# Kernel tuning notes

Hardware: AMD Instinct MI355X
Metric: run time of the kernel (lower is better)

The kernel has to match this reference:

```python
import jax, jax.numpy as jnp
import numpy as np

TAU = 0.6      # critical_fractile from params()
GAMMA = 0.1    # L2-regularization weight (init arg)
N_ITERS = 60   # bisection iterations (machine precision on [0,1])
EPS = 1e-12

# The cvxpy problem per sample (prob vector p over support y):
#   min_z  p @ pinball(y - z) + GAMMA * ||p * (y - z)||_2,   0 <= z <= 1
# with pinball(e) = max(TAU*e, (TAU-1)*e). This is a 1-D convex problem in z;
# we solve the stationarity condition g(z) = df/dz = 0 by bisection (g is
# nondecreasing), then take one Newton step at the root so implicit gradients
# w.r.t. p flow correctly (dz/dp = -(dg/dp)/(dg/dz)). Fully batched over B.

def setup_inputs() -> dict:
    key = jax.random.key(0)
    B, S = 32768, 1001
    x = jax.random.uniform(key, (B, S), dtype=jnp.float32)
    x = x / x.sum(-1, keepdims=True)                      # probability vectors
    y_supp = jnp.linspace(0.0, 1.0, S, dtype=jnp.float32)  # support grid
    return {"x": x, "y_supp": y_supp}


def _grad_z(z, p, y):
    """g(z)=df/dz and its z-derivative, batched. z:[B], p:[B,S], y:[S]."""
    e = y[None, :] - z[:, None]                                  # [B,S]
    pin = jnp.sum(p * jnp.where(e >= 0, -TAU, 1.0 - TAU), -1)    # d(pinball)/dz
    pe = p * e
    nrm = jnp.sqrt(jnp.sum(pe * pe, -1) + EPS)                   # ||p*e||
    s1 = jnp.sum(p * p * e, -1)
    g = pin - GAMMA * s1 / nrm
    gp = GAMMA * (jnp.sum(p * p, -1) / nrm - (s1 * s1) / (nrm ** 3))
    return g, gp


def _solve(x, y):
    B = x.shape[0]
    p0 = jax.lax.stop_gradient(x)
    y0 = jax.lax.stop_gradient(y)
    lo = jnp.zeros((B,), x.dtype)
    hi = jnp.ones((B,), x.dtype)

    def body(carry, _):
        lo, hi = carry
        mid = 0.5 * (lo + hi)
        g, _ = _grad_z(mid, p0, y0)
        lo = jnp.where(g < 0, mid, lo)
        hi = jnp.where(g < 0, hi, mid)
        return (lo, hi), None

    (lo, hi), _ = jax.lax.scan(body, (lo, hi), None, length=N_ITERS)
    z0 = jax.lax.stop_gradient(0.5 * (lo + hi))
    # one Newton step at the root -> correct implicit gradients w.r.t. x, y
    g, gp = _grad_z(z0, x, y)
    z = z0 - g / jnp.maximum(gp, 1e-8)
    # boundary clamp (minimum at 0 or 1 if g doesn't change sign)
    g0, _ = _grad_z(jnp.zeros((B,), x.dtype), p0, y0)
    g1, _ = _grad_z(jnp.ones((B,), x.dtype), p0, y0)
    z = jnp.where(g0 >= 0, 0.0, jnp.where(g1 <= 0, 1.0, jnp.clip(z, 0.0, 1.0)))
    return z


def reference(x, y_supp):
    z = _solve(x, y_supp)                   # [B]
    e = y_supp[None, :] - z[:, None]        # error variable, [B,S]
    pinball = jnp.maximum(TAU * e, (TAU - 1.0) * e)  # pinball_loss at optimum
    w_error = x * e                          # w_error variable
    return (z[:, None], pinball, e, w_error)
```

## Files before the change

kernel.cpp:

```cpp
#include <hip/hip_runtime.h>
#include <hip/hip_bf16.h>


constexpr int NS   = 1001;
constexpr int SPAD = 1024;
constexpr int NT   = 256;

__global__ __launch_bounds__(NT) void newsvendor_kernel(
    const float* __restrict__ x,
    const float* __restrict__ ysup,
    float* __restrict__ out,
    int B)
{
    __shared__ float  sp[SPAD];
    __shared__ float  sy[SPAD];
    __shared__ double scdf[SPAD];
    __shared__ double wred[12];
    __shared__ double wtot[4];
    __shared__ int    wredi[4];
    __shared__ double bc[4];
    __shared__ float  zf_sh;

    const int row  = blockIdx.x;
    const int tid  = threadIdx.x;
    const int lane = tid & 63;
    const int wv   = tid >> 6;
    const float* xr = x + (size_t)row * NS;

    for (int i = tid; i < SPAD; i += NT) {
        sp[i] = (i < NS) ? xr[i]   : 0.0f;
        sy[i] = (i < NS) ? ysup[i] : 2.0f;
    }
    __syncthreads();

    double a = 0.0, b1 = 0.0, c2 = 0.0;
    for (int i = tid; i < NS; i += NT) {
        double p = (double)sp[i], y = (double)sy[i];
        double pp = p * p;
        a += pp; b1 += pp * y; c2 += pp * (y * y);
    }
    for (int off = 32; off > 0; off >>= 1) {
        a  += __shfl_xor(a,  off);
        b1 += __shfl_xor(b1, off);
        c2 += __shfl_xor(c2, off);
    }
    if (lane == 0) { wred[wv*3+0] = a; wred[wv*3+1] = b1; wred[wv*3+2] = c2; }

    const int base = tid * 4;
    double p0 = sp[base], p1 = sp[base+1], p2 = sp[base+2], p3 = sp[base+3];
    double l0 = 0.0, l1 = p0, l2 = p0+p1, l3 = p0+p1+p2;
    double s  = p0+p1+p2+p3;
    double inc = s;
    for (int d = 1; d < 64; d <<= 1) {
        double t = __shfl_up(inc, (unsigned)d);
        if (lane >= d) inc += t;
    }
    if (lane == 63) wtot[wv] = inc;
    __syncthreads();

    double woff = 0.0;
    for (int w = 0; w < wv; ++w) woff += wtot[w];
    double ebase = woff + (inc - s);
    scdf[base]   = ebase + l0;
    scdf[base+1] = ebase + l1;
    scdf[base+2] = ebase + l2;
    scdf[base+3] = ebase + l3;
    if (tid == 0) {
        bc[0] = wred[0]+wred[3]+wred[6]+wred[9];
        bc[1] = wred[1]+wred[4]+wred[7]+wred[10];
        bc[2] = wred[2]+wred[5]+wred[8]+wred[11];
    }
    __syncthreads();

    const double A    = bc[0], B1 = bc[1], C = bc[2];
    const double Pt   = scdf[NS];
    const double ca   = (double)0.6f;
    const double cb   = (double)0.4f;
    const double cab  = ca + cb;
    const double GA   = (double)0.1f;
    const double GA2  = GA * GA;
    const double EPSd = (double)1e-12f;

    int kmin = 0x7fffffff;
    for (int k = tid; k < NS; k += NT) {
        double z  = (double)sy[k];
        double t  = cab * scdf[k] - ca * Pt;
        double s1 = B1 - z * A;
        double qe = C - z * (2.0 * B1 - z * A) + EPSd;
        double lq = t * t * qe, rq = GA2 * s1 * s1;
        bool ge = (t >= 0.0) ? (s1 <= 0.0 || lq >= rq)
                             : (s1 <  0.0 && lq <= rq);
        if (ge) kmin = min(kmin, k);
    }
    for (int off = 32; off > 0; off >>= 1)
        kmin = min(kmin, __shfl_xor(kmin, off));
    if (lane == 0) wredi[wv] = kmin;
    __syncthreads();

    if (tid == 0) {
        int kstar = min(min(wredi[0], wredi[1]), min(wredi[2], wredi[3]));

        double g0 = -ca * Pt - GA * B1 / sqrt(C + EPSd);
        int c1 = (sy[NS-1] < 1.0f) ? NS : NS - 1;
        double s1b = B1 - A;
        double qe1 = C - (2.0 * B1 - A) + EPSd;
        double g1 = cab * scdf[c1] - ca * Pt - GA * s1b / sqrt(qe1);

        float zf;
        if (g0 >= 0.0)      zf = 0.0f;
        else if (g1 <= 0.0) zf = 1.0f;
        else {
            int kk = kstar;
            float zlF, zrF;
            if (kk >= NS) { kk = NS; zlF = sy[NS-1]; zrF = 1.0f; }
            else {
                zlF = (kk > 0) ? sy[kk-1] : 0.0f;
                zrF = sy[kk];
            }
            double Phat = cab * scdf[kk] - ca * Pt;

            double zl  = (double)zlF;
            double s1l = B1 - zl * A;
            double qel = C - zl * (2.0 * B1 - zl * A) + EPSd;
            double lql = Phat * Phat * qel, rql = GA2 * s1l * s1l;
            bool Flge = (Phat >= 0.0) ? (s1l <= 0.0 || lql >= rql)
                                      : (s1l <  0.0 && lql <= rql);

            bool   jumpc;
            double zeta;
            if (Flge) { jumpc = true; zeta = zl; }
            else {
                jumpc = false;
                double E  = (C * A - B1 * B1) + A * EPSd;
                double cc = Phat / (GA * sqrt(A));
                double u  = cc * sqrt(E / fmax(1.0 - cc * cc, 1e-300));
                zeta = (B1 - u) / A;
                zeta = fmin(fmax(zeta, zl), (double)zrF);
            }

            float flo = 0.0f, fhi = 1.0f;
            for (int it = 0; it < 60; ++it) {
                float mid = 0.5f * (flo + fhi);
                bool dec = jumpc ? (mid <= zlF) : ((double)mid < zeta);
                if (dec) flo = mid; else fhi = mid;
            }
            float z0 = 0.5f * (flo + fhi);

            int cnt = (kk - 1) + ((zlF < z0) ? 1 : 0) + ((zrF < z0) ? 1 : 0);
            if (cnt < 0) cnt = 0;

            double z0d = (double)z0;
            double s1 = B1 - z0d * A;
            double qe = C - z0d * (2.0 * B1 - z0d * A) + EPSd;
            double nr = sqrt(qe);
            double inv = 1.0 / nr;
            double g  = cab * scdf[cnt] - ca * Pt - GA * s1 * inv;
            double gp = GA * inv * (A - s1 * s1 * (inv * inv));
            double zn = z0d - g / fmax(gp, (double)1e-8f);
            zn = fmin(fmax(zn, 0.0), 1.0);
            zf = (float)zn;
        }
        zf_sh = zf;
    }
    __syncthreads();

    const float zf = zf_sh;
    const size_t Bz = (size_t)B;
    const size_t rb = (size_t)row * NS;
    float* outPin = out + Bz + rb;
    float* outE   = out + Bz + Bz * NS + rb;
    float* outW   = out + Bz + 2 * Bz * NS + rb;
    if (tid == 0) out[row] = zf;
    for (int i = tid; i < NS; i += NT) {
        float e  = sy[i] - zf;
        float pb = fmaxf(0.6f * e, -0.4f * e);
        outPin[i] = pb;
        outE[i]   = e;
        outW[i]   = sp[i] * e;
    }
}

extern "C" void kernel_launch(void* const* d_in, const int* in_sizes, int n_in,
                              void* d_out, int out_size, void* d_ws, size_t ws_size,
                              hipStream_t stream)
{
    const float* x = (const float*)d_in[0];
    const float* y = (const float*)d_in[1];
    float* out = (float*)d_out;
    const int Ssz = in_sizes[1];
    const int B   = in_sizes[0] / Ssz;
    newsvendor_kernel<<<B, NT, 0, stream>>>(x, y, out, B);
}
```

Measured before the change: 551.4 us.

## Fuse reductions into per-thread float4 pass, pad scdf, drop a barrier, nontemporal stores

Each thread now loads its four elements of p and y once as float4 and computes both the moment sums and the prefix-scan inputs from those registers. The kink search evaluates those same four candidates from registers instead of re-reading shared memory. The bc broadcast and one __syncthreads are removed: every thread reads the warp partials directly. The scdf array is padded to avoid bank conflicts, the scalar bisection exits early at a float fixed point, and output writes use nontemporal stores. The kernel is dominated by memory traffic, so the compute-side savings may matter little. Nontemporal stores could help or hurt the write-back path.

```diff
diff --git a/kernel.cpp b/kernel.cpp
--- a/kernel.cpp
+++ b/kernel.cpp
@@ -2,9 +2,10 @@
 #include <hip/hip_bf16.h>
 
 
-constexpr int NS   = 1001;
-constexpr int SPAD = 1024;
-constexpr int NT   = 256;
+constexpr int NS = 1001;
+constexpr int SP = 1024;
+constexpr int NT = 256;
+#define SIDX(i) ((i) + ((i) >> 2))
 
 __global__ __launch_bounds__(NT) void newsvendor_kernel(
     const float* __restrict__ x,
@@ -12,13 +13,12 @@
     float* __restrict__ out,
     int B)
 {
-    __shared__ float  sp[SPAD];
-    __shared__ float  sy[SPAD];
-    __shared__ double scdf[SPAD];
+    __shared__ float  sp[SP];
+    __shared__ float  sy[SP];
+    __shared__ double scdf[SP + SP/4];
     __shared__ double wred[12];
     __shared__ double wtot[4];
     __shared__ int    wredi[4];
-    __shared__ double bc[4];
     __shared__ float  zf_sh;
 
     const int row  = blockIdx.x;
@@ -27,18 +27,26 @@
     const int wv   = tid >> 6;
     const float* xr = x + (size_t)row * NS;
 
-    for (int i = tid; i < SPAD; i += NT) {
+    #pragma unroll
+    for (int j = 0; j < 4; ++j) {
+        int i = tid + j * NT;
         sp[i] = (i < NS) ? xr[i]   : 0.0f;
         sy[i] = (i < NS) ? ysup[i] : 2.0f;
     }
     __syncthreads();
 
-    double a = 0.0, b1 = 0.0, c2 = 0.0;
-    for (int i = tid; i < NS; i += NT) {
-        double p = (double)sp[i], y = (double)sy[i];
-        double pp = p * p;
-        a += pp; b1 += pp * y; c2 += pp * (y * y);
-    }
+    const int base = tid * 4;
+    float4 pf = *reinterpret_cast<const float4*>(&sp[base]);
+    float4 yf = *reinterpret_cast<const float4*>(&sy[base]);
+    double p0 = pf.x, p1 = pf.y, p2 = pf.z, p3 = pf.w;
+    double y0d = yf.x, y1d = yf.y, y2d = yf.z, y3d = yf.w;
+    double q0 = p0*p0, q1 = p1*p1, q2 = p2*p2, q3 = p3*p3;
+    double a  = ((q0 + q1) + q2) + q3;
+    double b1 = ((q0*y0d + q1*y1d) + q2*y2d) + q3*y3d;
+    double c2 = ((q0*y0d*y0d + q1*y1d*y1d) + q2*y2d*y2d) + q3*y3d*y3d;
+    double l1 = p0, l2 = p0 + p1, l3 = l2 + p2;
+    double s  = l3 + p3;
+
     for (int off = 32; off > 0; off >>= 1) {
         a  += __shfl_xor(a,  off);
         b1 += __shfl_xor(b1, off);
@@ -46,10 +54,6 @@
     }
     if (lane == 0) { wred[wv*3+0] = a; wred[wv*3+1] = b1; wred[wv*3+2] = c2; }
 
-    const int base = tid * 4;
-    double p0 = sp[base], p1 = sp[base+1], p2 = sp[base+2], p3 = sp[base+3];
-    double l0 = 0.0, l1 = p0, l2 = p0+p1, l3 = p0+p1+p2;
-    double s  = p0+p1+p2+p3;
     double inc = s;
     for (int d = 1; d < 64; d <<= 1) {
         double t = __shfl_up(inc, (unsigned)d);
@@ -58,22 +62,19 @@
     if (lane == 63) wtot[wv] = inc;
     __syncthreads();
 
-    double woff = 0.0;
-    for (int w = 0; w < wv; ++w) woff += wtot[w];
-    double ebase = woff + (inc - s);
-    scdf[base]   = ebase + l0;
-    scdf[base+1] = ebase + l1;
-    scdf[base+2] = ebase + l2;
-    scdf[base+3] = ebase + l3;
-    if (tid == 0) {
-        bc[0] = wred[0]+wred[3]+wred[6]+wred[9];
-        bc[1] = wred[1]+wred[4]+wred[7]+wred[10];
-        bc[2] = wred[2]+wred[5]+wred[8]+wred[11];
-    }
-    __syncthreads();
-
-    const double A    = bc[0], B1 = bc[1], C = bc[2];
-    const double Pt   = scdf[NS];
+    const double w0 = wtot[0], w1 = wtot[1], w2 = wtot[2], w3 = wtot[3];
+    const double Pt = ((w0 + w1) + w2) + w3;
+    const double A  = wred[0] + wred[3] + wred[6] + wred[9];
+    const double B1 = wred[1] + wred[4] + wred[7] + wred[10];
+    const double C  = wred[2] + wred[5] + wred[8] + wred[11];
+    double woff = (wv > 0 ? w0 : 0.0) + (wv > 1 ? w1 : 0.0) + (wv > 2 ? w2 : 0.0);
+    double eb   = woff + (inc - s);
+    double sc0 = eb, sc1 = eb + l1, sc2 = eb + l2, sc3 = eb + l3;
+    scdf[SIDX(base+0)] = sc0;
+    scdf[SIDX(base+1)] = sc1;
+    scdf[SIDX(base+2)] = sc2;
+    scdf[SIDX(base+3)] = sc3;
+
     const double ca   = (double)0.6f;
     const double cb   = (double)0.4f;
     const double cab  = ca + cb;
@@ -82,15 +83,21 @@
     const double EPSd = (double)1e-12f;
 
     int kmin = 0x7fffffff;
-    for (int k = tid; k < NS; k += NT) {
-        double z  = (double)sy[k];
-        double t  = cab * scdf[k] - ca * Pt;
-        double s1 = B1 - z * A;
-        double qe = C - z * (2.0 * B1 - z * A) + EPSd;
-        double lq = t * t * qe, rq = GA2 * s1 * s1;
-        bool ge = (t >= 0.0) ? (s1 <= 0.0 || lq >= rq)
-                             : (s1 <  0.0 && lq <= rq);
-        if (ge) kmin = min(kmin, k);
+    {
+        double zz[4] = { y0d, y1d, y2d, y3d };
+        double cd[4] = { sc0, sc1, sc2, sc3 };
+        #pragma unroll
+        for (int j = 0; j < 4; ++j) {
+            int k = base + j;
+            double z  = zz[j];
+            double t  = cab * cd[j] - ca * Pt;
+            double s1 = B1 - z * A;
+            double qe = C - z * (2.0 * B1 - z * A) + EPSd;
+            double lq = t * t * qe, rq = GA2 * s1 * s1;
+            bool ge = (t >= 0.0) ? (s1 <= 0.0 || lq >= rq)
+                                 : (s1 <  0.0 && lq <= rq);
+            if (k < NS && ge) kmin = min(kmin, k);
+        }
     }
     for (int off = 32; off > 0; off >>= 1)
         kmin = min(kmin, __shfl_xor(kmin, off));
@@ -104,7 +111,7 @@
         int c1 = (sy[NS-1] < 1.0f) ? NS : NS - 1;
         double s1b = B1 - A;
         double qe1 = C - (2.0 * B1 - A) + EPSd;
-        double g1 = cab * scdf[c1] - ca * Pt - GA * s1b / sqrt(qe1);
+        double g1 = cab * scdf[SIDX(c1)] - ca * Pt - GA * s1b / sqrt(qe1);
 
         float zf;
         if (g0 >= 0.0)      zf = 0.0f;
@@ -117,7 +124,7 @@
                 zlF = (kk > 0) ? sy[kk-1] : 0.0f;
                 zrF = sy[kk];
             }
-            double Phat = cab * scdf[kk] - ca * Pt;
+            double Phat = cab * scdf[SIDX(kk)] - ca * Pt;
 
             double zl  = (double)zlF;
             double s1l = B1 - zl * A;
@@ -142,7 +149,9 @@
             for (int it = 0; it < 60; ++it) {
                 float mid = 0.5f * (flo + fhi);
                 bool dec = jumpc ? (mid <= zlF) : ((double)mid < zeta);
+                bool fixedpt = (mid == flo) || (mid == fhi);
                 if (dec) flo = mid; else fhi = mid;
+                if (fixedpt) break;
             }
             float z0 = 0.5f * (flo + fhi);
 
@@ -153,9 +162,9 @@
             double s1 = B1 - z0d * A;
             double qe = C - z0d * (2.0 * B1 - z0d * A) + EPSd;
             double nr = sqrt(qe);
-            double inv = 1.0 / nr;
-            double g  = cab * scdf[cnt] - ca * Pt - GA * s1 * inv;
-            double gp = GA * inv * (A - s1 * s1 * (inv * inv));
+            double invn = 1.0 / nr;
+            double g  = cab * scdf[SIDX(cnt)] - ca * Pt - GA * s1 * invn;
+            double gp = GA * invn * (A - s1 * s1 * (invn * invn));
             double zn = z0d - g / fmax(gp, (double)1e-8f);
             zn = fmin(fmax(zn, 0.0), 1.0);
             zf = (float)zn;
@@ -171,12 +180,16 @@
     float* outE   = out + Bz + Bz * NS + rb;
     float* outW   = out + Bz + 2 * Bz * NS + rb;
     if (tid == 0) out[row] = zf;
-    for (int i = tid; i < NS; i += NT) {
-        float e  = sy[i] - zf;
-        float pb = fmaxf(0.6f * e, -0.4f * e);
-        outPin[i] = pb;
-        outE[i]   = e;
-        outW[i]   = sp[i] * e;
+    #pragma unroll
+    for (int j = 0; j < 4; ++j) {
+        int i = tid + j * NT;
+        if (i < NS) {
+            float e  = sy[i] - zf;
+            float pb = fmaxf(0.6f * e, -0.4f * e);
+            __builtin_nontemporal_store(pb,        &outPin[i]);
+            __builtin_nontemporal_store(e,         &outE[i]);
+            __builtin_nontemporal_store(sp[i] * e, &outW[i]);
+        }
     }
 }
 
```

Measured after the change: 532.2 us. 3.5% less time.
